# Kernel optimization log

Measured on AMD Instinct MI355X. Metric: run time of the kernel, lower is better.

Reference implementation:

```python
import jax, jax.numpy as jnp
import numpy as np

V, E, H, ENC, ATT = 10000, 256, 512, 512, 512
B, S, NF, MAXLEN = 128, 25, 196, 64


def setup_inputs() -> dict:
    key = jax.random.key(0)
    ks = jax.random.split(key, 24)
    g = lambda k, shp: (jax.random.normal(k, shp, dtype=jnp.float32) * 0.05)
    emb = g(ks[0], (V, E)).at[0].set(0.0)  # padding_idx=0 row zeroed
    return {
        'decoder_input': jax.random.randint(ks[1], (B, S), 0, V, dtype=jnp.int32),
        'encoder_outputs': jax.random.normal(ks[2], (B, NF, ENC), dtype=jnp.float32),
        'emb': emb,
        'pos_emb': g(ks[3], (MAXLEN, E)),
        'Uw': g(ks[4], (ATT, ENC)), 'Ub': g(ks[5], (ATT,)),
        'Ww': g(ks[6], (ATT, H)), 'Wb': g(ks[7], (ATT,)),
        'Aw': g(ks[8], (1, ATT)), 'Ab': g(ks[9], (1,)),
        'init_h_w': g(ks[10], (H, ENC)), 'init_h_b': g(ks[11], (H,)),
        'init_c_w': g(ks[12], (H, ENC)), 'init_c_b': g(ks[13], (H,)),
        'W_ih': g(ks[14], (4 * H, E + ENC)), 'W_hh': g(ks[15], (4 * H, H)),
        'b_ih': g(ks[16], (4 * H,)), 'b_hh': g(ks[17], (4 * H,)),
        'fcn_w': g(ks[18], (V, H)), 'fcn_b': g(ks[19], (V,)),
    }


def reference(decoder_input, encoder_outputs, emb, pos_emb, Uw, Ub, Ww, Wb, Aw, Ab,
              init_h_w, init_h_b, init_c_w, init_c_b, W_ih, W_hh, b_ih, b_hh,
              fcn_w, fcn_b):
    # Loop-invariant attention key projection: U(features) -> [B, NF, ATT]
    u_hs = jnp.einsum('bne,ae->bna', encoder_outputs, Uw) + Ub
    mean_enc = encoder_outputs.mean(axis=1)                  # [B, ENC]
    h0 = mean_enc @ init_h_w.T + init_h_b                    # [B, H]
    c0 = mean_enc @ init_c_w.T + init_c_b
    tokens = decoder_input.T                                 # [S, B]
    positions = jnp.arange(tokens.shape[0])

    def step(carry, inp):
        h, c = carry
        tok, pos = inp
        embeds = emb[tok] + pos_emb[pos]                     # [B, E]
        w_ah = h @ Ww.T + Wb                                 # [B, ATT]
        scores = jnp.tanh(u_hs + w_ah[:, None, :]) @ Aw[0] + Ab[0]  # [B, NF]
        alpha = jax.nn.softmax(scores, axis=1)
        context = jnp.einsum('bnd,bn->bd', encoder_outputs, alpha)  # [B, ENC]
        x = jnp.concatenate([embeds, context], axis=1)       # [B, E+ENC]
        gates = x @ W_ih.T + b_ih + h @ W_hh.T + b_hh        # [B, 4H]
        i, f, g_, o = jnp.split(gates, 4, axis=1)
        c_new = jax.nn.sigmoid(f) * c + jax.nn.sigmoid(i) * jnp.tanh(g_)
        h_new = jax.nn.sigmoid(o) * jnp.tanh(c_new)
        out = h_new @ fcn_w.T + fcn_b                        # [B, V] (dropout=eval identity)
        return (h_new, c_new), (out, alpha)

    _, (outs, alphas) = jax.lax.scan(step, (h0, c0), (tokens, positions))
    return outs.transpose(1, 0, 2), alphas.transpose(1, 0, 2)
```

## Files before the change

kernel.cpp:

```cpp
#include <hip/hip_runtime.h>

constexpr int B_ = 128, S_ = 25, NF_ = 196, ENC_ = 512, ATT_ = 512;
constexpr int H_ = 512, E_ = 256, V_ = 10000, G4_ = 2048;
constexpr int VPAD_ = 10112;

typedef __attribute__((ext_vector_type(8))) __bf16 bf16x8;
typedef __attribute__((ext_vector_type(4))) __bf16 bf16x4;
typedef __attribute__((ext_vector_type(4))) float f32x4;

__device__ __forceinline__ float bflo(unsigned u) {
    return __builtin_bit_cast(float, u << 16);
}
__device__ __forceinline__ float bfhi(unsigned u) {
    return __builtin_bit_cast(float, u & 0xffff0000u);
}
__device__ __forceinline__ float fast_tanhf(float x) {
    x = fminf(fmaxf(x, -15.f), 15.f);
    return 1.f - 2.f * __fdividef(1.f, __expf(2.f * x) + 1.f);
}
__device__ __forceinline__ float fast_sigf(float x) {
    x = fminf(fmaxf(x, -30.f), 30.f);
    return __fdividef(1.f, 1.f + __expf(-x));
}

__device__ __forceinline__ int gperm(int n) {
    int j = (n & 15) + ((n >> 6) << 4);
    int g = (n >> 4) & 3;
    return g * 512 + j;
}

__global__ __launch_bounds__(256) void k_cvt(const float* __restrict__ s,
                                             __bf16* __restrict__ d, int n4) {
    int i = blockIdx.x * 256 + threadIdx.x;
    if (i >= n4) return;
    float4 v = *(const float4*)&s[(size_t)i * 4];
    bf16x4 o;
    o[0] = (__bf16)v.x; o[1] = (__bf16)v.y; o[2] = (__bf16)v.z; o[3] = (__bf16)v.w;
    *(bf16x4*)&d[(size_t)i * 4] = o;
}

__global__ __launch_bounds__(256) void k_cvt_fcw(const float* __restrict__ s,
                                                 __bf16* __restrict__ d) {
    int i = blockIdx.x * 256 + threadIdx.x;
    if (i >= VPAD_ * 512 / 4) return;
    int e = i * 4;
    int row = e >> 9;
    bf16x4 o;
    if (row < V_) {
        float4 v = *(const float4*)&s[(size_t)row * 512 + (e & 511)];
        o[0] = (__bf16)v.x; o[1] = (__bf16)v.y; o[2] = (__bf16)v.z; o[3] = (__bf16)v.w;
    } else {
        o[0] = o[1] = o[2] = o[3] = (__bf16)0.f;
    }
    *(bf16x4*)&d[(size_t)e] = o;
}

__global__ __launch_bounds__(256) void k_pack_ww(const float* __restrict__ Ww,
                                                 unsigned* __restrict__ W2) {
    __shared__ float Ts[32][65];
    int t = threadIdx.x;
    int k0 = blockIdx.x * 32, j0 = blockIdx.y * 64;
    int c = t & 31, rr = t >> 5;
#pragma unroll
    for (int i = 0; i < 8; ++i) {
        int j = j0 + rr + i * 8;
        Ts[c][rr + i * 8] = Ww[(size_t)j * 512 + k0 + c];
    }
    __syncthreads();
#pragma unroll
    for (int i = 0; i < 4; ++i) {
        int kr = (t >> 5) + i * 8;
        int jc = t & 31;
        __bf16 b0 = (__bf16)Ts[kr][2 * jc], b1 = (__bf16)Ts[kr][2 * jc + 1];
        unsigned u = (unsigned)__builtin_bit_cast(unsigned short, b0)
                   | ((unsigned)__builtin_bit_cast(unsigned short, b1) << 16);
        W2[(size_t)(k0 + kr) * 256 + (j0 >> 1) + jc] = u;
    }
}

__global__ __launch_bounds__(256) void k_cvt_wih_r(const float* __restrict__ W_ih,
                                                   __bf16* __restrict__ o) {
    int n = blockIdx.x, k = threadIdx.x;
    int row = gperm(n);
    o[(size_t)n * 256 + k] = (__bf16)W_ih[(size_t)row * 768 + k];
}

__global__ __launch_bounds__(256) void k_pack_wcat(const float* __restrict__ W_ih,
                                                   const float* __restrict__ W_hh,
                                                   __bf16* __restrict__ Wcat) {
    int n = blockIdx.x, t = threadIdx.x;
    int row = gperm(n);
#pragma unroll
    for (int i = 0; i < 4; ++i) {
        int k = t + i * 256;
        float v = (k < 512) ? W_ih[(size_t)row * 768 + 256 + k]
                            : W_hh[(size_t)row * 512 + (k - 512)];
        Wcat[(size_t)n * 1024 + k] = (__bf16)v;
    }
}

__global__ __launch_bounds__(256) void k_pack_biasr(const float* __restrict__ b_ih,
                                                    const float* __restrict__ b_hh,
                                                    float* __restrict__ bsum_r) {
    int n = blockIdx.x * 256 + threadIdx.x;
    int row = gperm(n);
    bsum_r[n] = b_ih[row] + b_hh[row];
}

__global__ __launch_bounds__(256) void k_embed(const int* __restrict__ dec,
                                               const float* __restrict__ emb,
                                               const float* __restrict__ pose,
                                               __bf16* __restrict__ out) {
    int bx = blockIdx.x;
    int s = bx >> 7, b = bx & 127;
    int e = threadIdx.x;
    int tok = dec[b * S_ + s];
    out[(size_t)bx * E_ + e] = (__bf16)(emb[tok * E_ + e] + pose[s * E_ + e]);
}

__global__ __launch_bounds__(1024) void k_init2(const float* __restrict__ enc,
                                                const float* __restrict__ ihw, const float* __restrict__ ihb,
                                                const float* __restrict__ icw, const float* __restrict__ icb,
                                                __bf16* __restrict__ Abuf0, float* __restrict__ cbuf) {
    __shared__ float pm[1024];
    __shared__ __align__(16) float mean[512];
    int b = blockIdx.x, t = threadIdx.x;
    int d = t & 511, q = t >> 9;
    const float* ep = enc + ((size_t)b * 196 + q * 98) * 512 + d;
    float sum = 0.f;
#pragma unroll 7
    for (int n = 0; n < 98; ++n) sum += ep[(size_t)n * 512];
    pm[t] = sum;
    __syncthreads();
    if (t < 512) mean[t] = (pm[t] + pm[t + 512]) * (1.f / 196.f);
    __syncthreads();
    int w = t >> 6, ln = t & 63;
    float4 m4a = *(const float4*)&mean[ln * 8];
    float4 m4b = *(const float4*)&mean[ln * 8 + 4];
#pragma unroll 4
    for (int i = 0; i < 32; ++i) {
        int j = i * 16 + w;
        const float4* wh = (const float4*)&ihw[(size_t)j * 512 + ln * 8];
        const float4* wc = (const float4*)&icw[(size_t)j * 512 + ln * 8];
        float4 ha = wh[0], hb = wh[1], ca = wc[0], cb = wc[1];
        float ah = m4a.x * ha.x + m4a.y * ha.y + m4a.z * ha.z + m4a.w * ha.w
                 + m4b.x * hb.x + m4b.y * hb.y + m4b.z * hb.z + m4b.w * hb.w;
        float ac = m4a.x * ca.x + m4a.y * ca.y + m4a.z * ca.z + m4a.w * ca.w
                 + m4b.x * cb.x + m4b.y * cb.y + m4b.z * cb.z + m4b.w * cb.w;
#pragma unroll
        for (int off = 32; off; off >>= 1) {
            ah += __shfl_xor(ah, off);
            ac += __shfl_xor(ac, off);
        }
        if (ln == 0) {
            Abuf0[(size_t)b * 1024 + 512 + j] = (__bf16)(ah + ihb[j]);
            cbuf[b * 512 + j] = ac + icb[j];
        }
    }
}

template<int MODE>
__global__ __launch_bounds__(256) void k_mfma_gemm(
    const __bf16* __restrict__ A, int lda, const __bf16* __restrict__ Bm,
    const float* __restrict__ bias1, void* __restrict__ Cout,
    int K, int Nreal, int ldc) {
    __shared__ __align__(16) __bf16 As[128 * 64];
    __shared__ __align__(16) __bf16 Bs[128 * 64];
    int tid = threadIdx.x;
    int lane = tid & 63, w = tid >> 6;
    int m0, n0;
    if (MODE == 0) {
        int nwg = gridDim.x * gridDim.y;
        int bid = blockIdx.y * gridDim.x + blockIdx.x;
        int q = nwg >> 3, r = nwg & 7;
        int xcd = bid & 7, lid = bid >> 3;
        int wgid = (xcd < r) ? xcd * (q + 1) + lid : r * (q + 1) + (xcd - r) * q + lid;
        m0 = (wgid % gridDim.x) * 128;
        n0 = (wgid / gridDim.x) * 128;
    } else {
        m0 = blockIdx.x * 128;
        n0 = blockIdx.y * 128;
    }
    int wm = (w & 1) * 64, wn = (w >> 1) * 64;
    f32x4 acc[4][4] = {};
    int srow = tid >> 3;
    int ke = (tid & 7) * 8;
    int kgw = tid & 7;

    for (int k0 = 0; k0 < K; k0 += 64) {
#pragma unroll
        for (int it = 0; it < 4; ++it) {
            int row = it * 32 + srow;
            bf16x8 av = *(const bf16x8*)(A + (size_t)(m0 + row) * lda + k0 + ke);
            bf16x8 bv = *(const bf16x8*)(Bm + (size_t)(n0 + row) * K + k0 + ke);
            int kg = kgw ^ (row & 7);
            *(bf16x8*)&As[row * 64 + kg * 8] = av;
            *(bf16x8*)&Bs[row * 64 + kg * 8] = bv;
        }
        __syncthreads();
        bf16x8 af[4][2], bfr[4][2];
#pragma unroll
        for (int f = 0; f < 4; ++f) {
#pragma unroll
            for (int ks = 0; ks < 2; ++ks) {
                int ra = wm + f * 16 + (lane & 15);
                int rb = wn + f * 16 + (lane & 15);
                int kgl = ks * 4 + (lane >> 4);
                af[f][ks]  = *(const bf16x8*)&As[ra * 64 + (kgl ^ (ra & 7)) * 8];
                bfr[f][ks] = *(const bf16x8*)&Bs[rb * 64 + (kgl ^ (rb & 7)) * 8];
            }
        }
#pragma unroll
        for (int fm = 0; fm < 4; ++fm)
#pragma unroll
            for (int fn = 0; fn < 4; ++fn)
#pragma unroll
                for (int ks = 0; ks < 2; ++ks)
                    acc[fm][fn] = __builtin_amdgcn_mfma_f32_16x16x32_bf16(
                        af[fm][ks], bfr[fn][ks], acc[fm][fn], 0, 0, 0);
        __syncthreads();
    }
    int cm = (lane >> 4) * 4, cn = lane & 15;
#pragma unroll
    for (int fm = 0; fm < 4; ++fm) {
#pragma unroll
        for (int fn = 0; fn < 4; ++fn) {
#pragma unroll
            for (int r = 0; r < 4; ++r) {
                int gm = m0 + wm + fm * 16 + cm + r;
                int gn = n0 + wn + fn * 16 + cn;
                float v = acc[fm][fn][r];
                if (MODE == 0) {
                    if (gn < Nreal) {
                        int orow = (gm & 127) * S_ + (gm >> 7);
                        ((float*)Cout)[(size_t)orow * ldc + gn] = v + bias1[gn];
                    }
                } else {
                    ((__bf16*)Cout)[(size_t)gm * ldc + gn] = (__bf16)(v + bias1[gn]);
                }
            }
        }
    }
}

__global__ __launch_bounds__(1024) void k_attn2(
    const __bf16* __restrict__ u_hs,
    const unsigned* __restrict__ enc2,
    const unsigned* __restrict__ W2,
    const float* __restrict__ Wb, const float* __restrict__ Aw,
    __bf16* __restrict__ Abuf,
    float* __restrict__ alphas, int s) {
    __shared__ __align__(16) float hs[512];
    __shared__ float wah[512];
    __shared__ float pc[2048];
    __shared__ float sc[200];
    int b = blockIdx.x, t = threadIdx.x;
    int ln = t & 63, w = t >> 6;

    if (t < 256) {
        unsigned u = ((const unsigned*)Abuf)[b * 512 + 256 + t];
        hs[2 * t] = bflo(u); hs[2 * t + 1] = bfhi(u);
    }
    __syncthreads();
    {
        int jp = t & 255, kq = t >> 8;
        float a0 = 0.f, a1 = 0.f;
        const unsigned* wp = W2 + (size_t)(kq * 128) * 256 + jp;
        const float4* h4 = (const float4*)(hs + kq * 128);
#pragma unroll 4
        for (int k4 = 0; k4 < 32; ++k4) {
            float4 hk = h4[k4];
            unsigned w0 = wp[(k4 * 4 + 0) * 256];
            unsigned w1 = wp[(k4 * 4 + 1) * 256];
            unsigned w2 = wp[(k4 * 4 + 2) * 256];
            unsigned w3 = wp[(k4 * 4 + 3) * 256];
            a0 += hk.x * bflo(w0); a1 += hk.x * bfhi(w0);
            a0 += hk.y * bflo(w1); a1 += hk.y * bfhi(w1);
            a0 += hk.z * bflo(w2); a1 += hk.z * bfhi(w2);
            a0 += hk.w * bflo(w3); a1 += hk.w * bfhi(w3);
        }
        pc[kq * 512 + 2 * jp] = a0;
        pc[kq * 512 + 2 * jp + 1] = a1;
    }
    __syncthreads();
    if (t < 512)
        wah[t] = pc[t] + pc[512 + t] + pc[1024 + t] + pc[1536 + t] + Wb[t];
    __syncthreads();
    {
        float av[8], wv[8];
#pragma unroll
        for (int i = 0; i < 8; ++i) { av[i] = Aw[ln * 8 + i]; wv[i] = wah[ln * 8 + i]; }
        for (int n = w; n < NF_; n += 16) {
            bf16x8 u8 = *(const bf16x8*)(u_hs + ((size_t)(b * NF_ + n)) * 512 + ln * 8);
            float acc = 0.f;
#pragma unroll
            for (int i = 0; i < 8; ++i)
                acc += fast_tanhf((float)u8[i] + wv[i]) * av[i];
#pragma unroll
            for (int off = 32; off; off >>= 1) acc += __shfl_xor(acc, off);
            if (ln == 0) sc[n] = __expf(acc);
        }
    }
    __syncthreads();
    float sum = sc[ln] + sc[ln + 64] + sc[ln + 128];
    if (ln < 4) sum += sc[ln + 192];
#pragma unroll
    for (int off = 32; off; off >>= 1) sum += __shfl_xor(sum, off);
    float inv = __fdividef(1.f, sum);
    if (t < NF_) alphas[((size_t)b * S_ + s) * NF_ + t] = sc[t] * inv;
    {
        int p2 = t & 255, q2 = t >> 8;
        float c0 = 0.f, c1 = 0.f;
        for (int i = q2; i < NF_; i += 4) {
            unsigned u = enc2[((size_t)(b * NF_ + i)) * 256 + p2];
            float a = sc[i];
            c0 += a * bflo(u); c1 += a * bfhi(u);
        }
        pc[q2 * 512 + 2 * p2] = c0;
        pc[q2 * 512 + 2 * p2 + 1] = c1;
    }
    __syncthreads();
    if (t < 512)
        Abuf[(size_t)b * 1024 + t] =
            (__bf16)((pc[t] + pc[512 + t] + pc[1024 + t] + pc[1536 + t]) * inv);
}

__global__ __launch_bounds__(256) void k_gates(
    const __bf16* __restrict__ Abuf,
    const __bf16* __restrict__ Wcat,
    const __bf16* __restrict__ gatespre,
    float* __restrict__ cbuf,
    __bf16* __restrict__ AbufN,
    __bf16* __restrict__ Hall_bf,
    int s) {
    __shared__ __align__(16) __bf16 As[2][32 * 64];
    __shared__ __align__(16) __bf16 Bs[2][64 * 64];
    __shared__ float Red[2048];
    int tid = threadIdx.x;
    int lane = tid & 63, w = tid >> 6;
    int m0 = blockIdx.x * 32, n0 = blockIdx.y * 64;
    int kh = w >> 1, wm = (w & 1) * 16;
    f32x4 acc[4] = {};
    int srow = tid >> 3;
    int ke = (tid & 7) * 8;
    int kgw = tid & 7;

    for (int k0 = 0; k0 < 512; k0 += 64) {
#pragma unroll
        for (int h = 0; h < 2; ++h) {
            int kb = h * 512 + k0;
            bf16x8 av = *(const bf16x8*)(Abuf + (size_t)(m0 + srow) * 1024 + kb + ke);
            int kg = kgw ^ (srow & 7);
            *(bf16x8*)&As[h][srow * 64 + kg * 8] = av;
#pragma unroll
            for (int it = 0; it < 2; ++it) {
                int row = it * 32 + srow;
                bf16x8 bv = *(const bf16x8*)(Wcat + (size_t)(n0 + row) * 1024 + kb + ke);
                int kg2 = kgw ^ (row & 7);
                *(bf16x8*)&Bs[h][row * 64 + kg2 * 8] = bv;
            }
        }
        __syncthreads();
        bf16x8 af[2], bfr[4][2];
#pragma unroll
        for (int ks = 0; ks < 2; ++ks) {
            int ra = wm + (lane & 15);
            int kgl = ks * 4 + (lane >> 4);
            af[ks] = *(const bf16x8*)&As[kh][ra * 64 + ((kgl ^ (ra & 7))) * 8];
#pragma unroll
            for (int fn = 0; fn < 4; ++fn) {
                int rb = fn * 16 + (lane & 15);
                bfr[fn][ks] = *(const bf16x8*)&Bs[kh][rb * 64 + ((kgl ^ (rb & 7))) * 8];
            }
        }
#pragma unroll
        for (int fn = 0; fn < 4; ++fn)
#pragma unroll
            for (int ks = 0; ks < 2; ++ks)
                acc[fn] = __builtin_amdgcn_mfma_f32_16x16x32_bf16(
                    af[ks], bfr[fn][ks], acc[fn], 0, 0, 0);
        __syncthreads();
    }
    int base = ((w & 1) * 64 + lane) * 16;
    if (kh == 1) {
#pragma unroll
        for (int fn = 0; fn < 4; ++fn)
#pragma unroll
            for (int r = 0; r < 4; ++r) Red[base + fn * 4 + r] = acc[fn][r];
    }
    __syncthreads();
    if (kh == 0) {
#pragma unroll
        for (int fn = 0; fn < 4; ++fn)
#pragma unroll
            for (int r = 0; r < 4; ++r) acc[fn][r] += Red[base + fn * 4 + r];
        int cm = (lane >> 4) * 4, cn = lane & 15;
        int j = (n0 >> 6) * 16 + cn;
#pragma unroll
        for (int r = 0; r < 4; ++r) {
            int b = m0 + wm + cm + r;
            const __bf16* gp = gatespre + ((size_t)(s * B_ + b)) * G4_ + n0 + cn;
            float qi = acc[0][r] + (float)gp[0];
            float qf = acc[1][r] + (float)gp[16];
            float qg = acc[2][r] + (float)gp[32];
            float qo = acc[3][r] + (float)gp[48];
            float ig = fast_sigf(qi), fg = fast_sigf(qf);
            float gg = fast_tanhf(qg), og = fast_sigf(qo);
            int ci = b * 512 + j;
            float cnew = fg * cbuf[ci] + ig * gg;
            float hn = og * fast_tanhf(cnew);
            cbuf[ci] = cnew;
            __bf16 hb = (__bf16)hn;
            AbufN[(size_t)b * 1024 + 512 + j] = hb;
            Hall_bf[(size_t)(s + 1) * 65536 + ci] = hb;
        }
    }
}

extern "C" void kernel_launch(void* const* d_in, const int* in_sizes, int n_in,
                              void* d_out, int out_size, void* d_ws, size_t ws_size,
                              hipStream_t stream) {
    const int*   dec  = (const int*)d_in[0];
    const float* enc  = (const float*)d_in[1];
    const float* emb  = (const float*)d_in[2];
    const float* pose = (const float*)d_in[3];
    const float* Uw   = (const float*)d_in[4];
    const float* Ub   = (const float*)d_in[5];
    const float* Ww   = (const float*)d_in[6];
    const float* Wb   = (const float*)d_in[7];
    const float* Aw   = (const float*)d_in[8];
    const float* ihw  = (const float*)d_in[10];
    const float* ihb  = (const float*)d_in[11];
    const float* icw  = (const float*)d_in[12];
    const float* icb  = (const float*)d_in[13];
    const float* W_ih = (const float*)d_in[14];
    const float* W_hh = (const float*)d_in[15];
    const float* b_ih = (const float*)d_in[16];
    const float* b_hh = (const float*)d_in[17];
    const float* fcw  = (const float*)d_in[18];
    const float* fcb  = (const float*)d_in[19];
    float* out = (float*)d_out;
    char*  wsb = (char*)d_ws;

    size_t o = 0;
    __bf16*   enc_bf   = (__bf16*)(wsb + o); o += (size_t)25088 * 512 * 2;
    __bf16*   u_hs_bf  = (__bf16*)(wsb + o); o += (size_t)25088 * 512 * 2;
    __bf16*   gpre_bf  = (__bf16*)(wsb + o); o += (size_t)3200 * 2048 * 2;
    __bf16*   Hall_bf  = (__bf16*)(wsb + o); o += (size_t)26 * 65536 * 2;
    float*    cbuf     = (float*)(wsb + o);  o += (size_t)65536 * 4;
    __bf16*   Abuf     = (__bf16*)(wsb + o); o += (size_t)2 * 128 * 1024 * 2;
    __bf16*   Uw_bf    = (__bf16*)(wsb + o); o += (size_t)262144 * 2;
    unsigned* W2       = (unsigned*)(wsb + o); o += (size_t)512 * 256 * 4;
    __bf16*   WihE_r   = (__bf16*)(wsb + o); o += (size_t)2048 * 256 * 2;
    __bf16*   embeds_bf= (__bf16*)(wsb + o); o += (size_t)3200 * 256 * 2;
    __bf16*   Wcat     = (__bf16*)(wsb + o); o += (size_t)2048 * 1024 * 2;
    float*    bsum_r   = (float*)(wsb + o);  o += (size_t)2048 * 4;
    __bf16*   fcw_bf   = (__bf16*)(wsb + o); o += (size_t)VPAD_ * 512 * 2;

    k_cvt<<<12544, 256, 0, stream>>>(enc, enc_bf, 3211264);
    k_cvt<<<256, 256, 0, stream>>>(Uw, Uw_bf, 65536);
    k_pack_ww<<<dim3(16, 8), 256, 0, stream>>>(Ww, W2);
    k_cvt_wih_r<<<2048, 256, 0, stream>>>(W_ih, WihE_r);
    k_pack_wcat<<<2048, 256, 0, stream>>>(W_ih, W_hh, Wcat);
    k_pack_biasr<<<8, 256, 0, stream>>>(b_ih, b_hh, bsum_r);
    k_embed<<<S_ * B_, 256, 0, stream>>>(dec, emb, pose, embeds_bf);
    k_init2<<<B_, 1024, 0, stream>>>(enc, ihw, ihb, icw, icb, Abuf, cbuf);
    k_cvt_fcw<<<5056, 256, 0, stream>>>(fcw, fcw_bf);

    k_mfma_gemm<1><<<dim3(196, 4), 256, 0, stream>>>(enc_bf, 512, Uw_bf, Ub,
                                                     u_hs_bf, 512, 512, 512);
    k_mfma_gemm<1><<<dim3(25, 16), 256, 0, stream>>>(embeds_bf, 256, WihE_r, bsum_r,
                                                     gpre_bf, 256, 2048, 2048);

    for (int s = 0; s < S_; ++s) {
        __bf16* Ap = Abuf + (size_t)(s & 1) * 131072;
        __bf16* An = Abuf + (size_t)((s + 1) & 1) * 131072;
        k_attn2<<<B_, 1024, 0, stream>>>(u_hs_bf, (const unsigned*)enc_bf, W2, Wb, Aw,
                                         Ap, out + 32000000, s);
        k_gates<<<dim3(4, 32), 256, 0, stream>>>(Ap, Wcat, gpre_bf, cbuf, An, Hall_bf, s);
    }

    k_mfma_gemm<0><<<dim3(25, 79), 256, 0, stream>>>(Hall_bf + 65536, 512, fcw_bf, fcb,
                                                     out, 512, V_, V_);
}
```

Baseline: 1.410 ms.

## Fuse attention and gate kernels per step with flag-based producer/consumer sync

Merges the per-step attention kernel and the LSTM gate kernel into one launch of 256 blocks. The first 128 blocks compute attention per batch row and publish a release flag. The other 128 blocks spin on the flags for their 32 batch rows before running the gate MFMA GEMM. This halves the per-step launch count and lets gate tiles start once their rows are ready. It relies on all 256 blocks being co-resident, and the 1024-thread launch bound wastes threads and occupancy in the gate blocks.

```diff
diff --git a/kernel.cpp b/kernel.cpp
--- a/kernel.cpp
+++ b/kernel.cpp
@@ -28,6 +28,8 @@
     int g = (n >> 4) & 3;
     return g * 512 + j;
 }
+
+__global__ __launch_bounds__(128) void k_zeroflags(int* flag) { flag[threadIdx.x] = 0; }
 
 __global__ __launch_bounds__(256) void k_cvt(const float* __restrict__ s,
                                              __bf16* __restrict__ d, int n4) {
@@ -243,176 +245,191 @@
     }
 }
 
-__global__ __launch_bounds__(1024) void k_attn2(
-    const __bf16* __restrict__ u_hs,
-    const unsigned* __restrict__ enc2,
-    const unsigned* __restrict__ W2,
-    const float* __restrict__ Wb, const float* __restrict__ Aw,
-    __bf16* __restrict__ Abuf,
-    float* __restrict__ alphas, int s) {
+__global__ __launch_bounds__(1024) void k_step(
+    const __bf16* __restrict__ u_hs, const unsigned* __restrict__ enc2,
+    const unsigned* __restrict__ W2, const float* __restrict__ Wb,
+    const float* __restrict__ Aw, const __bf16* __restrict__ Wcat,
+    const __bf16* __restrict__ gatespre, float* __restrict__ cbuf,
+    __bf16* __restrict__ Abuf, __bf16* __restrict__ AbufN,
+    __bf16* __restrict__ Hall_bf, float* __restrict__ alphas,
+    int* __restrict__ flag, int s) {
     __shared__ __align__(16) float hs[512];
     __shared__ float wah[512];
     __shared__ float pc[2048];
     __shared__ float sc[200];
-    int b = blockIdx.x, t = threadIdx.x;
-    int ln = t & 63, w = t >> 6;
-
-    if (t < 256) {
-        unsigned u = ((const unsigned*)Abuf)[b * 512 + 256 + t];
-        hs[2 * t] = bflo(u); hs[2 * t + 1] = bfhi(u);
-    }
-    __syncthreads();
-    {
-        int jp = t & 255, kq = t >> 8;
-        float a0 = 0.f, a1 = 0.f;
-        const unsigned* wp = W2 + (size_t)(kq * 128) * 256 + jp;
-        const float4* h4 = (const float4*)(hs + kq * 128);
+    __shared__ __align__(16) __bf16 Asg[2][32 * 64];
+    __shared__ __align__(16) __bf16 Bsg[2][64 * 64];
+    __shared__ float Red[2048];
+
+    int bid = blockIdx.x, t = threadIdx.x;
+
+    if (bid < 128) {
+        int b = bid;
+        int ln = t & 63, w = t >> 6;
+        if (t < 256) {
+            unsigned u = ((const unsigned*)Abuf)[b * 512 + 256 + t];
+            hs[2 * t] = bflo(u); hs[2 * t + 1] = bfhi(u);
+        }
+        __syncthreads();
+        {
+            int jp = t & 255, kq = t >> 8;
+            float a0 = 0.f, a1 = 0.f;
+            const unsigned* wp = W2 + (size_t)(kq * 128) * 256 + jp;
+            const float4* h4 = (const float4*)(hs + kq * 128);
 #pragma unroll 4
-        for (int k4 = 0; k4 < 32; ++k4) {
-            float4 hk = h4[k4];
-            unsigned w0 = wp[(k4 * 4 + 0) * 256];
-            unsigned w1 = wp[(k4 * 4 + 1) * 256];
-            unsigned w2 = wp[(k4 * 4 + 2) * 256];
-            unsigned w3 = wp[(k4 * 4 + 3) * 256];
-            a0 += hk.x * bflo(w0); a1 += hk.x * bfhi(w0);
-            a0 += hk.y * bflo(w1); a1 += hk.y * bfhi(w1);
-            a0 += hk.z * bflo(w2); a1 += hk.z * bfhi(w2);
-            a0 += hk.w * bflo(w3); a1 += hk.w * bfhi(w3);
-        }
-        pc[kq * 512 + 2 * jp] = a0;
-        pc[kq * 512 + 2 * jp + 1] = a1;
-    }
-    __syncthreads();
-    if (t < 512)
-        wah[t] = pc[t] + pc[512 + t] + pc[1024 + t] + pc[1536 + t] + Wb[t];
-    __syncthreads();
-    {
-        float av[8], wv[8];
-#pragma unroll
-        for (int i = 0; i < 8; ++i) { av[i] = Aw[ln * 8 + i]; wv[i] = wah[ln * 8 + i]; }
-        for (int n = w; n < NF_; n += 16) {
-            bf16x8 u8 = *(const bf16x8*)(u_hs + ((size_t)(b * NF_ + n)) * 512 + ln * 8);
-            float acc = 0.f;
-#pragma unroll
-            for (int i = 0; i < 8; ++i)
-                acc += fast_tanhf((float)u8[i] + wv[i]) * av[i];
-#pragma unroll
-            for (int off = 32; off; off >>= 1) acc += __shfl_xor(acc, off);
-            if (ln == 0) sc[n] = __expf(acc);
-        }
-    }
-    __syncthreads();
-    float sum = sc[ln] + sc[ln + 64] + sc[ln + 128];
-    if (ln < 4) sum += sc[ln + 192];
-#pragma unroll
-    for (int off = 32; off; off >>= 1) sum += __shfl_xor(sum, off);
-    float inv = __fdividef(1.f, sum);
-    if (t < NF_) alphas[((size_t)b * S_ + s) * NF_ + t] = sc[t] * inv;
-    {
-        int p2 = t & 255, q2 = t >> 8;
-        float c0 = 0.f, c1 = 0.f;
-        for (int i = q2; i < NF_; i += 4) {
-            unsigned u = enc2[((size_t)(b * NF_ + i)) * 256 + p2];
-            float a = sc[i];
-            c0 += a * bflo(u); c1 += a * bfhi(u);
-        }
-        pc[q2 * 512 + 2 * p2] = c0;
-        pc[q2 * 512 + 2 * p2 + 1] = c1;
-    }
-    __syncthreads();
-    if (t < 512)
-        Abuf[(size_t)b * 1024 + t] =
-            (__bf16)((pc[t] + pc[512 + t] + pc[1024 + t] + pc[1536 + t]) * inv);
-}
-
-__global__ __launch_bounds__(256) void k_gates(
-    const __bf16* __restrict__ Abuf,
-    const __bf16* __restrict__ Wcat,
-    const __bf16* __restrict__ gatespre,
-    float* __restrict__ cbuf,
-    __bf16* __restrict__ AbufN,
-    __bf16* __restrict__ Hall_bf,
-    int s) {
-    __shared__ __align__(16) __bf16 As[2][32 * 64];
-    __shared__ __align__(16) __bf16 Bs[2][64 * 64];
-    __shared__ float Red[2048];
-    int tid = threadIdx.x;
-    int lane = tid & 63, w = tid >> 6;
-    int m0 = blockIdx.x * 32, n0 = blockIdx.y * 64;
-    int kh = w >> 1, wm = (w & 1) * 16;
-    f32x4 acc[4] = {};
-    int srow = tid >> 3;
-    int ke = (tid & 7) * 8;
-    int kgw = tid & 7;
-
-    for (int k0 = 0; k0 < 512; k0 += 64) {
-#pragma unroll
-        for (int h = 0; h < 2; ++h) {
-            int kb = h * 512 + k0;
-            bf16x8 av = *(const bf16x8*)(Abuf + (size_t)(m0 + srow) * 1024 + kb + ke);
-            int kg = kgw ^ (srow & 7);
-            *(bf16x8*)&As[h][srow * 64 + kg * 8] = av;
-#pragma unroll
-            for (int it = 0; it < 2; ++it) {
-                int row = it * 32 + srow;
-                bf16x8 bv = *(const bf16x8*)(Wcat + (size_t)(n0 + row) * 1024 + kb + ke);
-                int kg2 = kgw ^ (row & 7);
-                *(bf16x8*)&Bs[h][row * 64 + kg2 * 8] = bv;
-            }
-        }
-        __syncthreads();
-        bf16x8 af[2], bfr[4][2];
-#pragma unroll
-        for (int ks = 0; ks < 2; ++ks) {
-            int ra = wm + (lane & 15);
-            int kgl = ks * 4 + (lane >> 4);
-            af[ks] = *(const bf16x8*)&As[kh][ra * 64 + ((kgl ^ (ra & 7))) * 8];
-#pragma unroll
-            for (int fn = 0; fn < 4; ++fn) {
-                int rb = fn * 16 + (lane & 15);
-                bfr[fn][ks] = *(const bf16x8*)&Bs[kh][rb * 64 + ((kgl ^ (rb & 7))) * 8];
-            }
-        }
-#pragma unroll
-        for (int fn = 0; fn < 4; ++fn)
-#pragma unroll
-            for (int ks = 0; ks < 2; ++ks)
-                acc[fn] = __builtin_amdgcn_mfma_f32_16x16x32_bf16(
-                    af[ks], bfr[fn][ks], acc[fn], 0, 0, 0);
-        __syncthreads();
-    }
-    int base = ((w & 1) * 64 + lane) * 16;
-    if (kh == 1) {
-#pragma unroll
-        for (int fn = 0; fn < 4; ++fn)
-#pragma unroll
-            for (int r = 0; r < 4; ++r) Red[base + fn * 4 + r] = acc[fn][r];
-    }
-    __syncthreads();
-    if (kh == 0) {
-#pragma unroll
-        for (int fn = 0; fn < 4; ++fn)
-#pragma unroll
-            for (int r = 0; r < 4; ++r) acc[fn][r] += Red[base + fn * 4 + r];
-        int cm = (lane >> 4) * 4, cn = lane & 15;
-        int j = (n0 >> 6) * 16 + cn;
-#pragma unroll
-        for (int r = 0; r < 4; ++r) {
-            int b = m0 + wm + cm + r;
-            const __bf16* gp = gatespre + ((size_t)(s * B_ + b)) * G4_ + n0 + cn;
-            float qi = acc[0][r] + (float)gp[0];
-            float qf = acc[1][r] + (float)gp[16];
-            float qg = acc[2][r] + (float)gp[32];
-            float qo = acc[3][r] + (float)gp[48];
-            float ig = fast_sigf(qi), fg = fast_sigf(qf);
-            float gg = fast_tanhf(qg), og = fast_sigf(qo);
-            int ci = b * 512 + j;
-            float cnew = fg * cbuf[ci] + ig * gg;
-            float hn = og * fast_tanhf(cnew);
-            cbuf[ci] = cnew;
-            __bf16 hb = (__bf16)hn;
-            AbufN[(size_t)b * 1024 + 512 + j] = hb;
-            Hall_bf[(size_t)(s + 1) * 65536 + ci] = hb;
+            for (int k4 = 0; k4 < 32; ++k4) {
+                float4 hk = h4[k4];
+                unsigned w0 = wp[(k4 * 4 + 0) * 256];
+                unsigned w1 = wp[(k4 * 4 + 1) * 256];
+                unsigned w2 = wp[(k4 * 4 + 2) * 256];
+                unsigned w3 = wp[(k4 * 4 + 3) * 256];
+                a0 += hk.x * bflo(w0); a1 += hk.x * bfhi(w0);
+                a0 += hk.y * bflo(w1); a1 += hk.y * bfhi(w1);
+                a0 += hk.z * bflo(w2); a1 += hk.z * bfhi(w2);
+                a0 += hk.w * bflo(w3); a1 += hk.w * bfhi(w3);
+            }
+            pc[kq * 512 + 2 * jp] = a0;
+            pc[kq * 512 + 2 * jp + 1] = a1;
+        }
+        __syncthreads();
+        if (t < 512)
+            wah[t] = pc[t] + pc[512 + t] + pc[1024 + t] + pc[1536 + t] + Wb[t];
+        __syncthreads();
+        {
+            float av[8], wv[8];
+#pragma unroll
+            for (int i = 0; i < 8; ++i) { av[i] = Aw[ln * 8 + i]; wv[i] = wah[ln * 8 + i]; }
+            for (int n = w; n < NF_; n += 16) {
+                bf16x8 u8 = *(const bf16x8*)(u_hs + ((size_t)(b * NF_ + n)) * 512 + ln * 8);
+                float acc = 0.f;
+#pragma unroll
+                for (int i = 0; i < 8; ++i)
+                    acc += fast_tanhf((float)u8[i] + wv[i]) * av[i];
+#pragma unroll
+                for (int off = 32; off; off >>= 1) acc += __shfl_xor(acc, off);
+                if (ln == 0) sc[n] = __expf(acc);
+            }
+        }
+        __syncthreads();
+        float sum = sc[ln] + sc[ln + 64] + sc[ln + 128];
+        if (ln < 4) sum += sc[ln + 192];
+#pragma unroll
+        for (int off = 32; off; off >>= 1) sum += __shfl_xor(sum, off);
+        float inv = __fdividef(1.f, sum);
+        if (t < NF_) alphas[((size_t)b * S_ + s) * NF_ + t] = sc[t] * inv;
+        {
+            int p2 = t & 255, q2 = t >> 8;
+            float c0 = 0.f, c1 = 0.f;
+            for (int i = q2; i < NF_; i += 4) {
+                unsigned u = enc2[((size_t)(b * NF_ + i)) * 256 + p2];
+                float a = sc[i];
+                c0 += a * bflo(u); c1 += a * bfhi(u);
+            }
+            pc[q2 * 512 + 2 * p2] = c0;
+            pc[q2 * 512 + 2 * p2 + 1] = c1;
+        }
+        __syncthreads();
+        if (t < 512)
+            Abuf[(size_t)b * 1024 + t] =
+                (__bf16)((pc[t] + pc[512 + t] + pc[1024 + t] + pc[1536 + t]) * inv);
+        __syncthreads();
+        if (t == 0) {
+            __threadfence();
+            __hip_atomic_store(&flag[b], s + 1, __ATOMIC_RELEASE, __HIP_MEMORY_SCOPE_AGENT);
+        }
+    } else {
+        if (t >= 256) return;
+        int gbk = bid - 128;
+        int m0 = (gbk & 3) * 32, n0 = (gbk >> 2) * 64;
+        if (t < 64) {
+            int ln = t;
+            for (;;) {
+                int v = (ln < 32)
+                    ? __hip_atomic_load(&flag[m0 + ln], __ATOMIC_ACQUIRE, __HIP_MEMORY_SCOPE_AGENT)
+                    : 0x7fffffff;
+                if (__all(v >= s + 1)) break;
+                __builtin_amdgcn_s_sleep(2);
+            }
+        }
+        __syncthreads();
+
+        int tid = t;
+        int lane = tid & 63, w = tid >> 6;
+        int kh = w >> 1, wm = (w & 1) * 16;
+        f32x4 acc[4] = {};
+        int srow = tid >> 3;
+        int ke = (tid & 7) * 8;
+        int kgw = tid & 7;
+
+        for (int k0 = 0; k0 < 512; k0 += 64) {
+#pragma unroll
+            for (int h = 0; h < 2; ++h) {
+                int kb = h * 512 + k0;
+                bf16x8 av = *(const bf16x8*)(Abuf + (size_t)(m0 + srow) * 1024 + kb + ke);
+                int kg = kgw ^ (srow & 7);
+                *(bf16x8*)&Asg[h][srow * 64 + kg * 8] = av;
+#pragma unroll
+                for (int it = 0; it < 2; ++it) {
+                    int row = it * 32 + srow;
+                    bf16x8 bv = *(const bf16x8*)(Wcat + (size_t)(n0 + row) * 1024 + kb + ke);
+                    int kg2 = kgw ^ (row & 7);
+                    *(bf16x8*)&Bsg[h][row * 64 + kg2 * 8] = bv;
+                }
+            }
+            __syncthreads();
+            bf16x8 af[2], bfr[4][2];
+#pragma unroll
+            for (int ks = 0; ks < 2; ++ks) {
+                int ra = wm + (lane & 15);
+                int kgl = ks * 4 + (lane >> 4);
+                af[ks] = *(const bf16x8*)&Asg[kh][ra * 64 + ((kgl ^ (ra & 7))) * 8];
+#pragma unroll
+                for (int fn = 0; fn < 4; ++fn) {
+                    int rb = fn * 16 + (lane & 15);
+                    bfr[fn][ks] = *(const bf16x8*)&Bsg[kh][rb * 64 + ((kgl ^ (rb & 7))) * 8];
+                }
+            }
+#pragma unroll
+            for (int fn = 0; fn < 4; ++fn)
+#pragma unroll
+                for (int ks = 0; ks < 2; ++ks)
+                    acc[fn] = __builtin_amdgcn_mfma_f32_16x16x32_bf16(
+                        af[ks], bfr[fn][ks], acc[fn], 0, 0, 0);
+            __syncthreads();
+        }
+        int base = ((w & 1) * 64 + lane) * 16;
+        if (kh == 1) {
+#pragma unroll
+            for (int fn = 0; fn < 4; ++fn)
+#pragma unroll
+                for (int r = 0; r < 4; ++r) Red[base + fn * 4 + r] = acc[fn][r];
+        }
+        __syncthreads();
+        if (kh == 0) {
+#pragma unroll
+            for (int fn = 0; fn < 4; ++fn)
+#pragma unroll
+                for (int r = 0; r < 4; ++r) acc[fn][r] += Red[base + fn * 4 + r];
+            int cm = (lane >> 4) * 4, cn = lane & 15;
+            int j = (n0 >> 6) * 16 + cn;
+#pragma unroll
+            for (int r = 0; r < 4; ++r) {
+                int b = m0 + wm + cm + r;
+                const __bf16* gp = gatespre + ((size_t)(s * B_ + b)) * G4_ + n0 + cn;
+                float qi = acc[0][r] + (float)gp[0];
+                float qf = acc[1][r] + (float)gp[16];
+                float qg = acc[2][r] + (float)gp[32];
+                float qo = acc[3][r] + (float)gp[48];
+                float ig = fast_sigf(qi), fg = fast_sigf(qf);
+                float gg = fast_tanhf(qg), og = fast_sigf(qo);
+                int ci = b * 512 + j;
+                float cnew = fg * cbuf[ci] + ig * gg;
+                float hn = og * fast_tanhf(cnew);
+                cbuf[ci] = cnew;
+                __bf16 hb = (__bf16)hn;
+                AbufN[(size_t)b * 1024 + 512 + j] = hb;
+                Hall_bf[(size_t)(s + 1) * 65536 + ci] = hb;
+            }
         }
     }
 }
@@ -456,7 +473,9 @@
     __bf16*   Wcat     = (__bf16*)(wsb + o); o += (size_t)2048 * 1024 * 2;
     float*    bsum_r   = (float*)(wsb + o);  o += (size_t)2048 * 4;
     __bf16*   fcw_bf   = (__bf16*)(wsb + o); o += (size_t)VPAD_ * 512 * 2;
-
+    int*      flags    = (int*)(wsb + o);    o += 128 * 4;
+
+    k_zeroflags<<<1, 128, 0, stream>>>(flags);
     k_cvt<<<12544, 256, 0, stream>>>(enc, enc_bf, 3211264);
     k_cvt<<<256, 256, 0, stream>>>(Uw, Uw_bf, 65536);
     k_pack_ww<<<dim3(16, 8), 256, 0, stream>>>(Ww, W2);
@@ -475,9 +494,9 @@
     for (int s = 0; s < S_; ++s) {
         __bf16* Ap = Abuf + (size_t)(s & 1) * 131072;
         __bf16* An = Abuf + (size_t)((s + 1) & 1) * 131072;
-        k_attn2<<<B_, 1024, 0, stream>>>(u_hs_bf, (const unsigned*)enc_bf, W2, Wb, Aw,
-                                         Ap, out + 32000000, s);
-        k_gates<<<dim3(4, 32), 256, 0, stream>>>(Ap, Wcat, gpre_bf, cbuf, An, Hall_bf, s);
+        k_step<<<256, 1024, 0, stream>>>(u_hs_bf, (const unsigned*)enc_bf, W2, Wb, Aw,
+                                         Wcat, gpre_bf, cbuf, Ap, An, Hall_bf,
+                                         out + 32000000, flags, s);
     }
 
     k_mfma_gemm<0><<<dim3(25, 79), 256, 0, stream>>>(Hall_bf + 65536, 512, fcw_bf, fcb,
```

New measurement: 2.939 ms. 2.08x slower.

## Merge setup kernels, batch pre-GEMMs, and stage FCN epilogue through LDS

Applied to the files above, without the earlier changes.

Folds the nine preprocessing kernels into one block-indexed setup kernel and the two independent pre-loop GEMMs into one launch, which cuts launch count and lets the small jobs share the GPU. The final vocab projection now writes its accumulators to shared memory in 32-row chunks and stores them as coalesced float4 rows with bias added, instead of scattered scalar stores. In exchange the fused kernels branch on block index, and the FCN epilogue adds extra syncs and LDS round trips.

```diff
diff --git a/kernel.cpp b/kernel.cpp
--- a/kernel.cpp
+++ b/kernel.cpp
@@ -29,93 +29,91 @@
     return g * 512 + j;
 }
 
-__global__ __launch_bounds__(256) void k_cvt(const float* __restrict__ s,
-                                             __bf16* __restrict__ d, int n4) {
-    int i = blockIdx.x * 256 + threadIdx.x;
-    if (i >= n4) return;
-    float4 v = *(const float4*)&s[(size_t)i * 4];
-    bf16x4 o;
-    o[0] = (__bf16)v.x; o[1] = (__bf16)v.y; o[2] = (__bf16)v.z; o[3] = (__bf16)v.w;
-    *(bf16x4*)&d[(size_t)i * 4] = o;
-}
-
-__global__ __launch_bounds__(256) void k_cvt_fcw(const float* __restrict__ s,
-                                                 __bf16* __restrict__ d) {
-    int i = blockIdx.x * 256 + threadIdx.x;
-    if (i >= VPAD_ * 512 / 4) return;
-    int e = i * 4;
-    int row = e >> 9;
-    bf16x4 o;
-    if (row < V_) {
-        float4 v = *(const float4*)&s[(size_t)row * 512 + (e & 511)];
+__global__ __launch_bounds__(256) void k_setup(
+    const float* __restrict__ enc, __bf16* __restrict__ enc_bf,
+    const float* __restrict__ Uw, __bf16* __restrict__ Uw_bf,
+    const float* __restrict__ Ww, unsigned* __restrict__ W2,
+    const float* __restrict__ W_ih, __bf16* __restrict__ WihE_r,
+    const float* __restrict__ W_hh, __bf16* __restrict__ Wcat,
+    const float* __restrict__ b_ih, const float* __restrict__ b_hh,
+    float* __restrict__ bsum_r,
+    const int* __restrict__ dec, const float* __restrict__ emb,
+    const float* __restrict__ pose, __bf16* __restrict__ embeds_bf,
+    const float* __restrict__ fcw, __bf16* __restrict__ fcw_bf) {
+    __shared__ float Ts[32][65];
+    int bid = blockIdx.x, t = threadIdx.x;
+
+    if (bid < 12544) {
+        int i = bid * 256 + t;
+        if (i < 3211264) {
+            float4 v = *(const float4*)&enc[(size_t)i * 4];
+            bf16x4 o;
+            o[0] = (__bf16)v.x; o[1] = (__bf16)v.y; o[2] = (__bf16)v.z; o[3] = (__bf16)v.w;
+            *(bf16x4*)&enc_bf[(size_t)i * 4] = o;
+        }
+    } else if (bid < 12800) {
+        int i = (bid - 12544) * 256 + t;
+        float4 v = *(const float4*)&Uw[(size_t)i * 4];
+        bf16x4 o;
         o[0] = (__bf16)v.x; o[1] = (__bf16)v.y; o[2] = (__bf16)v.z; o[3] = (__bf16)v.w;
+        *(bf16x4*)&Uw_bf[(size_t)i * 4] = o;
+    } else if (bid < 12928) {
+        int l = bid - 12800;
+        int k0 = (l & 15) * 32, j0 = (l >> 4) * 64;
+        int c = t & 31, rr = t >> 5;
+#pragma unroll
+        for (int i = 0; i < 8; ++i) {
+            int j = j0 + rr + i * 8;
+            Ts[c][rr + i * 8] = Ww[(size_t)j * 512 + k0 + c];
+        }
+        __syncthreads();
+#pragma unroll
+        for (int i = 0; i < 4; ++i) {
+            int kr = (t >> 5) + i * 8;
+            int jc = t & 31;
+            __bf16 b0 = (__bf16)Ts[kr][2 * jc], b1 = (__bf16)Ts[kr][2 * jc + 1];
+            unsigned u = (unsigned)__builtin_bit_cast(unsigned short, b0)
+                       | ((unsigned)__builtin_bit_cast(unsigned short, b1) << 16);
+            W2[(size_t)(k0 + kr) * 256 + (j0 >> 1) + jc] = u;
+        }
+    } else if (bid < 14976) {
+        int n = bid - 12928;
+        int row = gperm(n);
+        WihE_r[(size_t)n * 256 + t] = (__bf16)W_ih[(size_t)row * 768 + t];
+    } else if (bid < 17024) {
+        int n = bid - 14976;
+        int row = gperm(n);
+#pragma unroll
+        for (int i = 0; i < 4; ++i) {
+            int k = t + i * 256;
+            float v = (k < 512) ? W_ih[(size_t)row * 768 + 256 + k]
+                                : W_hh[(size_t)row * 512 + (k - 512)];
+            Wcat[(size_t)n * 1024 + k] = (__bf16)v;
+        }
+    } else if (bid < 17032) {
+        int n = (bid - 17024) * 256 + t;
+        int row = gperm(n);
+        bsum_r[n] = b_ih[row] + b_hh[row];
+    } else if (bid < 20232) {
+        int bx = bid - 17032;
+        int s = bx >> 7, b = bx & 127;
+        int tok = dec[b * S_ + s];
+        embeds_bf[(size_t)bx * E_ + t] = (__bf16)(emb[tok * E_ + t] + pose[s * E_ + t]);
     } else {
-        o[0] = o[1] = o[2] = o[3] = (__bf16)0.f;
-    }
-    *(bf16x4*)&d[(size_t)e] = o;
-}
-
-__global__ __launch_bounds__(256) void k_pack_ww(const float* __restrict__ Ww,
-                                                 unsigned* __restrict__ W2) {
-    __shared__ float Ts[32][65];
-    int t = threadIdx.x;
-    int k0 = blockIdx.x * 32, j0 = blockIdx.y * 64;
-    int c = t & 31, rr = t >> 5;
-#pragma unroll
-    for (int i = 0; i < 8; ++i) {
-        int j = j0 + rr + i * 8;
-        Ts[c][rr + i * 8] = Ww[(size_t)j * 512 + k0 + c];
-    }
-    __syncthreads();
-#pragma unroll
-    for (int i = 0; i < 4; ++i) {
-        int kr = (t >> 5) + i * 8;
-        int jc = t & 31;
-        __bf16 b0 = (__bf16)Ts[kr][2 * jc], b1 = (__bf16)Ts[kr][2 * jc + 1];
-        unsigned u = (unsigned)__builtin_bit_cast(unsigned short, b0)
-                   | ((unsigned)__builtin_bit_cast(unsigned short, b1) << 16);
-        W2[(size_t)(k0 + kr) * 256 + (j0 >> 1) + jc] = u;
-    }
-}
-
-__global__ __launch_bounds__(256) void k_cvt_wih_r(const float* __restrict__ W_ih,
-                                                   __bf16* __restrict__ o) {
-    int n = blockIdx.x, k = threadIdx.x;
-    int row = gperm(n);
-    o[(size_t)n * 256 + k] = (__bf16)W_ih[(size_t)row * 768 + k];
-}
-
-__global__ __launch_bounds__(256) void k_pack_wcat(const float* __restrict__ W_ih,
-                                                   const float* __restrict__ W_hh,
-                                                   __bf16* __restrict__ Wcat) {
-    int n = blockIdx.x, t = threadIdx.x;
-    int row = gperm(n);
-#pragma unroll
-    for (int i = 0; i < 4; ++i) {
-        int k = t + i * 256;
-        float v = (k < 512) ? W_ih[(size_t)row * 768 + 256 + k]
-                            : W_hh[(size_t)row * 512 + (k - 512)];
-        Wcat[(size_t)n * 1024 + k] = (__bf16)v;
-    }
-}
-
-__global__ __launch_bounds__(256) void k_pack_biasr(const float* __restrict__ b_ih,
-                                                    const float* __restrict__ b_hh,
-                                                    float* __restrict__ bsum_r) {
-    int n = blockIdx.x * 256 + threadIdx.x;
-    int row = gperm(n);
-    bsum_r[n] = b_ih[row] + b_hh[row];
-}
-
-__global__ __launch_bounds__(256) void k_embed(const int* __restrict__ dec,
-                                               const float* __restrict__ emb,
-                                               const float* __restrict__ pose,
-                                               __bf16* __restrict__ out) {
-    int bx = blockIdx.x;
-    int s = bx >> 7, b = bx & 127;
-    int e = threadIdx.x;
-    int tok = dec[b * S_ + s];
-    out[(size_t)bx * E_ + e] = (__bf16)(emb[tok * E_ + e] + pose[s * E_ + e]);
+        int i = (bid - 20232) * 256 + t;
+        if (i < VPAD_ * 512 / 4) {
+            int e = i * 4;
+            int row = e >> 9;
+            bf16x4 o;
+            if (row < V_) {
+                float4 v = *(const float4*)&fcw[(size_t)row * 512 + (e & 511)];
+                o[0] = (__bf16)v.x; o[1] = (__bf16)v.y; o[2] = (__bf16)v.z; o[3] = (__bf16)v.w;
+            } else {
+                o[0] = o[1] = o[2] = o[3] = (__bf16)0.f;
+            }
+            *(bf16x4*)&fcw_bf[(size_t)e] = o;
+        }
+    }
 }
 
 __global__ __launch_bounds__(1024) void k_init2(const float* __restrict__ enc,
@@ -159,28 +157,27 @@
     }
 }
 
-template<int MODE>
-__global__ __launch_bounds__(256) void k_mfma_gemm(
-    const __bf16* __restrict__ A, int lda, const __bf16* __restrict__ Bm,
-    const float* __restrict__ bias1, void* __restrict__ Cout,
-    int K, int Nreal, int ldc) {
+__global__ __launch_bounds__(256) void k_gemms(
+    const __bf16* __restrict__ Aa, const __bf16* __restrict__ Ba,
+    const float* __restrict__ ba, __bf16* __restrict__ Ca,
+    const __bf16* __restrict__ Ab, const __bf16* __restrict__ Bb,
+    const float* __restrict__ bb, __bf16* __restrict__ Cb) {
     __shared__ __align__(16) __bf16 As[128 * 64];
     __shared__ __align__(16) __bf16 Bs[128 * 64];
-    int tid = threadIdx.x;
+    int bid = blockIdx.x, tid = threadIdx.x;
+    const __bf16 *A, *Bm;
+    const float* bias;
+    __bf16* C;
+    int lda, K, ldc, m0, n0;
+    if (bid < 784) {
+        A = Aa; Bm = Ba; bias = ba; C = Ca; lda = 512; K = 512; ldc = 512;
+        m0 = (bid % 196) * 128; n0 = (bid / 196) * 128;
+    } else {
+        int i = bid - 784;
+        A = Ab; Bm = Bb; bias = bb; C = Cb; lda = 256; K = 256; ldc = 2048;
+        m0 = (i % 25) * 128; n0 = (i / 25) * 128;
+    }
     int lane = tid & 63, w = tid >> 6;
-    int m0, n0;
-    if (MODE == 0) {
-        int nwg = gridDim.x * gridDim.y;
-        int bid = blockIdx.y * gridDim.x + blockIdx.x;
-        int q = nwg >> 3, r = nwg & 7;
-        int xcd = bid & 7, lid = bid >> 3;
-        int wgid = (xcd < r) ? xcd * (q + 1) + lid : r * (q + 1) + (xcd - r) * q + lid;
-        m0 = (wgid % gridDim.x) * 128;
-        n0 = (wgid / gridDim.x) * 128;
-    } else {
-        m0 = blockIdx.x * 128;
-        n0 = blockIdx.y * 128;
-    }
     int wm = (w & 1) * 64, wn = (w >> 1) * 64;
     f32x4 acc[4][4] = {};
     int srow = tid >> 3;
@@ -222,24 +219,109 @@
     }
     int cm = (lane >> 4) * 4, cn = lane & 15;
 #pragma unroll
-    for (int fm = 0; fm < 4; ++fm) {
-#pragma unroll
-        for (int fn = 0; fn < 4; ++fn) {
+    for (int fm = 0; fm < 4; ++fm)
+#pragma unroll
+        for (int fn = 0; fn < 4; ++fn)
 #pragma unroll
             for (int r = 0; r < 4; ++r) {
                 int gm = m0 + wm + fm * 16 + cm + r;
                 int gn = n0 + wn + fn * 16 + cn;
-                float v = acc[fm][fn][r];
-                if (MODE == 0) {
-                    if (gn < Nreal) {
-                        int orow = (gm & 127) * S_ + (gm >> 7);
-                        ((float*)Cout)[(size_t)orow * ldc + gn] = v + bias1[gn];
-                    }
-                } else {
-                    ((__bf16*)Cout)[(size_t)gm * ldc + gn] = (__bf16)(v + bias1[gn]);
-                }
-            }
-        }
+                C[(size_t)gm * ldc + gn] = (__bf16)(acc[fm][fn][r] + bias[gn]);
+            }
+}
+
+__global__ __launch_bounds__(256) void k_fcn(
+    const __bf16* __restrict__ A, const __bf16* __restrict__ Bm,
+    const float* __restrict__ bias1, float* __restrict__ Cout) {
+    __shared__ __align__(16) __bf16 As[128 * 64];
+    __shared__ __align__(16) __bf16 Bs[128 * 64];
+    int tid = threadIdx.x;
+    int lane = tid & 63, w = tid >> 6;
+    int nwg = gridDim.x * gridDim.y;
+    int bid = blockIdx.y * gridDim.x + blockIdx.x;
+    int q = nwg >> 3, r0 = nwg & 7;
+    int xcd = bid & 7, lid = bid >> 3;
+    int wgid = (xcd < r0) ? xcd * (q + 1) + lid : r0 * (q + 1) + (xcd - r0) * q + lid;
+    int m0 = (wgid % gridDim.x) * 128;
+    int n0 = (wgid / gridDim.x) * 128;
+
+    int wm = (w & 1) * 64, wn = (w >> 1) * 64;
+    f32x4 acc[4][4] = {};
+    int srow = tid >> 3;
+    int ke = (tid & 7) * 8;
+    int kgw = tid & 7;
+
+    for (int k0 = 0; k0 < 512; k0 += 64) {
+#pragma unroll
+        for (int it = 0; it < 4; ++it) {
+            int row = it * 32 + srow;
+            bf16x8 av = *(const bf16x8*)(A + (size_t)(m0 + row) * 512 + k0 + ke);
+            bf16x8 bv = *(const bf16x8*)(Bm + (size_t)(n0 + row) * 512 + k0 + ke);
+            int kg = kgw ^ (row & 7);
+            *(bf16x8*)&As[row * 64 + kg * 8] = av;
+            *(bf16x8*)&Bs[row * 64 + kg * 8] = bv;
+        }
+        __syncthreads();
+        bf16x8 af[4][2], bfr[4][2];
+#pragma unroll
+        for (int f = 0; f < 4; ++f) {
+#pragma unroll
+            for (int ks = 0; ks < 2; ++ks) {
+                int ra = wm + f * 16 + (lane & 15);
+                int rb = wn + f * 16 + (lane & 15);
+                int kgl = ks * 4 + (lane >> 4);
+                af[f][ks]  = *(const bf16x8*)&As[ra * 64 + (kgl ^ (ra & 7)) * 8];
+                bfr[f][ks] = *(const bf16x8*)&Bs[rb * 64 + (kgl ^ (rb & 7)) * 8];
+            }
+        }
+#pragma unroll
+        for (int fm = 0; fm < 4; ++fm)
+#pragma unroll
+            for (int fn = 0; fn < 4; ++fn)
+#pragma unroll
+                for (int ks = 0; ks < 2; ++ks)
+                    acc[fm][fn] = __builtin_amdgcn_mfma_f32_16x16x32_bf16(
+                        af[fm][ks], bfr[fn][ks], acc[fm][fn], 0, 0, 0);
+        __syncthreads();
+    }
+    float* LDSf = (float*)As;
+    int cm = (lane >> 4) * 4, cn = lane & 15;
+#pragma unroll
+    for (int c = 0; c < 4; ++c) {
+        if ((w & 1) == (c >> 1)) {
+            int fmb = (c & 1) * 2;
+#pragma unroll
+            for (int fi = 0; fi < 2; ++fi) {
+                int fm = fmb + fi;
+#pragma unroll
+                for (int fn = 0; fn < 4; ++fn)
+#pragma unroll
+                    for (int r = 0; r < 4; ++r)
+                        LDSf[(fi * 16 + cm + r) * 128 + wn + fn * 16 + cn] = acc[fm][fn][r];
+            }
+        }
+        __syncthreads();
+        int row = tid >> 3, cb = (tid & 7) * 16;
+        int grow = m0 + c * 32 + row;
+        int orow = (grow & 127) * S_ + (grow >> 7);
+        float* dst = Cout + (size_t)orow * V_;
+#pragma unroll
+        for (int qq = 0; qq < 4; ++qq) {
+            int gn = n0 + cb + qq * 4;
+            float4 v;
+            v.x = LDSf[row * 128 + cb + qq * 4 + 0] + ((gn + 0 < V_) ? bias1[gn + 0] : 0.f);
+            v.y = LDSf[row * 128 + cb + qq * 4 + 1] + ((gn + 1 < V_) ? bias1[gn + 1] : 0.f);
+            v.z = LDSf[row * 128 + cb + qq * 4 + 2] + ((gn + 2 < V_) ? bias1[gn + 2] : 0.f);
+            v.w = LDSf[row * 128 + cb + qq * 4 + 3] + ((gn + 3 < V_) ? bias1[gn + 3] : 0.f);
+            if (gn + 3 < V_) {
+                *(float4*)&dst[gn] = v;
+            } else {
+                if (gn + 0 < V_) dst[gn + 0] = v.x;
+                if (gn + 1 < V_) dst[gn + 1] = v.y;
+                if (gn + 2 < V_) dst[gn + 2] = v.z;
+            }
+        }
+        __syncthreads();
     }
 }
 
@@ -457,20 +539,13 @@
     float*    bsum_r   = (float*)(wsb + o);  o += (size_t)2048 * 4;
     __bf16*   fcw_bf   = (__bf16*)(wsb + o); o += (size_t)VPAD_ * 512 * 2;
 
-    k_cvt<<<12544, 256, 0, stream>>>(enc, enc_bf, 3211264);
-    k_cvt<<<256, 256, 0, stream>>>(Uw, Uw_bf, 65536);
-    k_pack_ww<<<dim3(16, 8), 256, 0, stream>>>(Ww, W2);
-    k_cvt_wih_r<<<2048, 256, 0, stream>>>(W_ih, WihE_r);
-    k_pack_wcat<<<2048, 256, 0, stream>>>(W_ih, W_hh, Wcat);
-    k_pack_biasr<<<8, 256, 0, stream>>>(b_ih, b_hh, bsum_r);
-    k_embed<<<S_ * B_, 256, 0, stream>>>(dec, emb, pose, embeds_bf);
+    k_setup<<<25288, 256, 0, stream>>>(enc, enc_bf, Uw, Uw_bf, Ww, W2,
+                                       W_ih, WihE_r, W_hh, Wcat,
+                                       b_ih, b_hh, bsum_r,
+                                       dec, emb, pose, embeds_bf, fcw, fcw_bf);
     k_init2<<<B_, 1024, 0, stream>>>(enc, ihw, ihb, icw, icb, Abuf, cbuf);
-    k_cvt_fcw<<<5056, 256, 0, stream>>>(fcw, fcw_bf);
-
-    k_mfma_gemm<1><<<dim3(196, 4), 256, 0, stream>>>(enc_bf, 512, Uw_bf, Ub,
-                                                     u_hs_bf, 512, 512, 512);
-    k_mfma_gemm<1><<<dim3(25, 16), 256, 0, stream>>>(embeds_bf, 256, WihE_r, bsum_r,
-                                                     gpre_bf, 256, 2048, 2048);
+    k_gemms<<<1184, 256, 0, stream>>>(enc_bf, Uw_bf, Ub, u_hs_bf,
+                                      embeds_bf, WihE_r, bsum_r, gpre_bf);
 
     for (int s = 0; s < S_; ++s) {
         __bf16* Ap = Abuf + (size_t)(s & 1) * 131072;
@@ -480,6 +555,5 @@
         k_gates<<<dim3(4, 32), 256, 0, stream>>>(Ap, Wcat, gpre_bf, cbuf, An, Hall_bf, s);
     }
 
-    k_mfma_gemm<0><<<dim3(25, 79), 256, 0, stream>>>(Hall_bf + 65536, 512, fcw_bf, fcb,
-                                                     out, 512, V_, V_);
-}
+    k_fcn<<<dim3(25, 79), 256, 0, stream>>>(Hall_bf + 65536, fcw_bf, fcb, out);
+}
```

Result: no change. 1.410 ms (+0.0%).
